# Performance work log

Hardware: AMD Instinct MI355X
Metric: run time of the kernel (lower is better)

The kernel has to match this reference:

```python
import jax, jax.numpy as jnp
import numpy as np

EPS = 1e-5  # 'eps' forward arg, fixed as in typical transformer LayerNorm


def setup_inputs() -> dict:
    key = jax.random.key(0)
    ks = jax.random.split(key, 9)
    B, S, D = 4, 2048, 2048
    scale = 0.02
    return {
        "inputs": jax.random.normal(ks[0], (B, S, D), jnp.float32),
        "norm_weight": jax.random.uniform(ks[1], (D,), jnp.float32),
        "norm_bias": jax.random.normal(ks[2], (D,), jnp.float32) * scale,
        "q_weight": jax.random.normal(ks[3], (D, D), jnp.float32) * scale,
        "q_bias": jax.random.normal(ks[4], (D,), jnp.float32) * scale,
        "k_weight": jax.random.normal(ks[5], (D, D), jnp.float32) * scale,
        "k_bias": jax.random.normal(ks[6], (D,), jnp.float32) * scale,
        "v_weight": jax.random.normal(ks[7], (D, D), jnp.float32) * scale,
        "v_bias": jax.random.normal(ks[8], (D,), jnp.float32) * scale,
        "trans_b": 1,
        "shape_param": 0,
    }


def _layernorm(x, w, b, eps):
    mu = jnp.mean(x, axis=-1, keepdims=True)
    var = jnp.mean(jnp.square(x - mu), axis=-1, keepdims=True)
    return (x - mu) * jax.lax.rsqrt(var + eps) * w + b


def reference(inputs, norm_weight, norm_bias, q_weight, q_bias,
              k_weight, k_bias, v_weight, v_bias, trans_b, shape_param):
    # fused LayerNorm + Q/K/V projection (torch_mlu_ops.fused_norm_attention_project)
    normed = _layernorm(inputs, norm_weight, norm_bias, EPS)
    # trans_b==True convention: weights are [out, in] (nn.Linear layout)
    if not trans_b:
        q_weight = q_weight.T
        k_weight = None if k_weight is None else k_weight.T
        v_weight = None if v_weight is None else v_weight.T
    q = jnp.einsum('bsd,od->bso', normed, q_weight) + q_bias
    outs = [q]
    if k_weight is not None:
        outs.append(jnp.einsum('bsd,od->bso', normed, k_weight) + k_bias)
    if v_weight is not None:
        outs.append(jnp.einsum('bsd,od->bso', normed, v_weight) + v_bias)
    output = jnp.concatenate(outs, axis=-1)  # [B, S, 3*D] fused QKV
    if shape_param:
        output = output.reshape(shape_param)
    return output
```

## Files before the change

kernel.cpp:

```cpp
#include <hip/hip_runtime.h>
#include <hip/hip_bf16.h>
#include <stdint.h>

__device__ __forceinline__ uint16_t f2bf(float f) {
    union { float f; uint32_t u; } c; c.f = f;
    uint32_t u = c.u;
    return (uint16_t)((u + 0x7FFFu + ((u >> 16) & 1u)) >> 16);
}
__device__ __forceinline__ uint32_t pack2(float a, float b) {
    return (uint32_t)f2bf(a) | ((uint32_t)f2bf(b) << 16);
}

typedef __bf16 bf16x8 __attribute__((ext_vector_type(8)));
typedef float  f32x4  __attribute__((ext_vector_type(4)));

#define GLOAD_LDS16(g, l) __builtin_amdgcn_global_load_lds( \
    (const __attribute__((address_space(1))) void*)(g),     \
    (__attribute__((address_space(3))) void*)(l), 16, 0, 0)

#define FENCE() asm volatile("" ::: "memory")

__global__ __launch_bounds__(256) void ln_kernel(
    const float* __restrict__ x, const float* __restrict__ gw,
    const float* __restrict__ gb, uint16_t* __restrict__ y, int D)
{
    const int t = threadIdx.x;
    const size_t row = blockIdx.x;
    const float4* xr = (const float4*)(x + row * (size_t)D);
    float4 v0 = xr[2 * t], v1 = xr[2 * t + 1];

    float s  = v0.x + v0.y + v0.z + v0.w + v1.x + v1.y + v1.z + v1.w;
    float ss = v0.x * v0.x + v0.y * v0.y + v0.z * v0.z + v0.w * v0.w
             + v1.x * v1.x + v1.y * v1.y + v1.z * v1.z + v1.w * v1.w;
#pragma unroll
    for (int off = 32; off > 0; off >>= 1) {
        s  += __shfl_down(s, off);
        ss += __shfl_down(ss, off);
    }
    __shared__ float red[10];
    const int wave = t >> 6, lane = t & 63;
    if (lane == 0) { red[wave] = s; red[4 + wave] = ss; }
    __syncthreads();
    if (t == 0) {
        float S  = red[0] + red[1] + red[2] + red[3];
        float SS = red[4] + red[5] + red[6] + red[7];
        float mu = S / (float)D;
        float var = SS / (float)D - mu * mu;
        red[8] = mu;
        red[9] = rsqrtf(var + 1e-5f);
    }
    __syncthreads();
    const float mu = red[8], rstd = red[9];

    const float4* wr = (const float4*)gw;
    const float4* br = (const float4*)gb;
    float4 w0 = wr[2 * t], w1 = wr[2 * t + 1];
    float4 b0 = br[2 * t], b1 = br[2 * t + 1];

    uint4 ov;
    ov.x = pack2((v0.x - mu) * rstd * w0.x + b0.x, (v0.y - mu) * rstd * w0.y + b0.y);
    ov.y = pack2((v0.z - mu) * rstd * w0.z + b0.z, (v0.w - mu) * rstd * w0.w + b0.w);
    ov.z = pack2((v1.x - mu) * rstd * w1.x + b1.x, (v1.y - mu) * rstd * w1.y + b1.y);
    ov.w = pack2((v1.z - mu) * rstd * w1.z + b1.z, (v1.w - mu) * rstd * w1.w + b1.w);
    ((uint4*)(y + row * (size_t)D))[t] = ov;
}

__global__ __launch_bounds__(256) void wcvt_kernel(
    const float* __restrict__ wq, const float* __restrict__ wk,
    const float* __restrict__ wv, uint16_t* __restrict__ out)
{
    const size_t i = ((size_t)blockIdx.x * 256 + threadIdx.x) * 8;
    const int which = (int)(i >> 22);
    const float* src = (which == 0) ? wq : (which == 1) ? wk : wv;
    const size_t off = i & ((1u << 22) - 1);
    float4 a = *(const float4*)(src + off);
    float4 b = *(const float4*)(src + off + 4);
    uint4 ov;
    ov.x = pack2(a.x, a.y);
    ov.y = pack2(a.z, a.w);
    ov.z = pack2(b.x, b.y);
    ov.w = pack2(b.z, b.w);
    *(uint4*)(out + i) = ov;
}


#define STAGE_A(H, KT, SL) do {                                               \
    const uint16_t* g_ = gA + (size_t)((H) * 128) * K + (KT) * 64;            \
    char* l_ = (char*)lds + (((SL) * 2 + (H)) * 16384) + t * 16;              \
    GLOAD_LDS16(g_, l_);                                                      \
    GLOAD_LDS16(g_ + (size_t)64 * K, l_ + 8192);                              \
} while (0)

#define STAGE_B(H, KT, SL) do {                                               \
    const uint16_t* g_ = gB + (size_t)((H) * 128) * K + (KT) * 64;            \
    char* l_ = (char*)lds + 65536 + (((SL) * 2 + (H)) * 16384) + t * 16;      \
    GLOAD_LDS16(g_, l_);                                                      \
    GLOAD_LDS16(g_ + (size_t)64 * K, l_ + 8192);                              \
} while (0)

#define DS_READ_A(buf, P)                                                     \
    _Pragma("unroll") for (int m_ = 0; m_ < 2; ++m_)                          \
      _Pragma("unroll") for (int s_ = 0; s_ < 2; ++s_)                        \
        buf[m_][s_] = *(const bf16x8*)((const char*)lds + ab_                 \
                                       + (aoff ^ (s_ << 6))                   \
                                       + (2 * (P) + m_) * 2048);

#define DS_READ_BF()                                                          \
    _Pragma("unroll") for (int j_ = 0; j_ < 4; ++j_)                          \
      _Pragma("unroll") for (int s_ = 0; s_ < 2; ++s_)                        \
        Bf[j_][s_] = *(const bf16x8*)((const char*)lds + bb_                  \
                                      + (boff ^ (s_ << 6)) + j_ * 2048);

#define MFMA16(P, buf)                                                        \
    __builtin_amdgcn_s_setprio(1);                                            \
    _Pragma("unroll") for (int s_ = 0; s_ < 2; ++s_)                          \
      _Pragma("unroll") for (int m_ = 0; m_ < 2; ++m_)                        \
        _Pragma("unroll") for (int j_ = 0; j_ < 4; ++j_)                      \
          acc[2 * (P) + m_][j_] = __builtin_amdgcn_mfma_f32_16x16x32_bf16(    \
              buf[m_][s_], Bf[j_][s_], acc[2 * (P) + m_][j_], 0, 0, 0);       \
    __builtin_amdgcn_s_setprio(0);

#define KTILE(SLOT, KT, SA, SB, TAILWAIT)                                     \
  {                                                                           \
    const int ab_ = ((SLOT) * 2 + wr) * 16384;                                \
    const int bb_ = 65536 + ((SLOT) * 2 + (wc >> 1)) * 16384;                 \
    bf16x8 Bf[4][2], AfA[2][2], AfB[2][2];                                    \
                                                                      \
    DS_READ_BF(); DS_READ_A(AfA, 0); DS_READ_A(AfB, 1);                       \
    if (SA) STAGE_A(0, (KT) + 1, (SLOT) ^ 1);                                 \
    FENCE();                                                                  \
    __builtin_amdgcn_s_barrier();                                             \
    MFMA16(0, AfA);                                                           \
    __builtin_amdgcn_s_barrier();                                             \
    FENCE();                                                                  \
                                                                      \
    DS_READ_A(AfA, 2);                                                        \
    if (SA) STAGE_A(1, (KT) + 1, (SLOT) ^ 1);                                 \
    FENCE();                                                                  \
    __builtin_amdgcn_s_barrier();                                             \
    MFMA16(1, AfB);                                                           \
    __builtin_amdgcn_s_barrier();                                             \
    FENCE();                                                                  \
                                                                      \
    DS_READ_A(AfB, 3);                                                        \
    if (SB) STAGE_B(0, (KT) + 2, (SLOT));                                     \
    FENCE();                                                                  \
    __builtin_amdgcn_s_barrier();                                             \
    MFMA16(2, AfA);                                                           \
    __builtin_amdgcn_s_barrier();                                             \
    FENCE();                                                                  \
                                                                      \
    if (SB) STAGE_B(1, (KT) + 2, (SLOT));                                     \
    FENCE();                                                                  \
    __builtin_amdgcn_s_barrier();                                             \
    MFMA16(3, AfB);                                                           \
    TAILWAIT                                                                  \
    __builtin_amdgcn_s_barrier();                                             \
    FENCE();                                                                  \
  }

__global__ __launch_bounds__(512, 2) void qkv_gemm256(
    const uint16_t* __restrict__ A, const uint16_t* __restrict__ W,
    const float* __restrict__ Bq, const float* __restrict__ Bk,
    const float* __restrict__ Bv, float* __restrict__ C,
    int M, int N, int K)
{
    (void)M;
    extern __shared__ uint16_t lds[];
    const int t = threadIdx.x;
    const int lane = t & 63, wid = t >> 6;
    const int wr = wid >> 2, wc = wid & 3;
    const int fr = lane & 15;
    const int fq2 = (lane >> 4) * 16;

    const int nbt = N >> 8;
    const int nwg = gridDim.x;
    int mb, nb;
    if ((nwg & 7) == 0) {
        const int cpx = nwg >> 3;
        const int xcd = blockIdx.x & 7, ti = blockIdx.x >> 3;
        if (cpx % nbt == 0 && (nbt & 7) == 0) {
            const int band = ti >> 5, r = ti & 31;
            mb = xcd * (cpx / nbt) + (r >> 3);
            nb = (band << 3) + (r & 7);
        } else {
            const int swz = xcd * cpx + ti;
            mb = swz / nbt; nb = swz % nbt;
        }
    } else {
        mb = blockIdx.x / nbt; nb = blockIdx.x % nbt;
    }

    const int kbase = fq2 ^ ((fr & 7) << 4);
    const int aoff = fr * 128 + kbase;
    const int boff = ((wc & 1) * 64 + fr) * 128 + kbase;

    const int srow = t >> 3;
    const int scol = (((t & 7) ^ ((t >> 3) & 7)) << 3);
    const uint16_t* gA = A + (size_t)(mb * 256 + srow) * K + scol;
    const uint16_t* gB = W + (size_t)(nb * 256 + srow) * K + scol;

    f32x4 acc[8][4] = {};
    const int NT = K >> 6;

    STAGE_B(0, 0, 0); STAGE_B(1, 0, 0);
    STAGE_A(0, 0, 0); STAGE_A(1, 0, 0);
    STAGE_B(0, 1, 1); STAGE_B(1, 1, 1);
    asm volatile("s_waitcnt vmcnt(4)" ::: "memory");
    __builtin_amdgcn_s_barrier();
    FENCE();

#pragma unroll 1
    for (int i = 0; i < (NT >> 1) - 1; ++i) {
        const int k0 = i << 1;
        KTILE(0, k0,     1, 1, asm volatile("s_waitcnt vmcnt(4)" ::: "memory");)
        KTILE(1, k0 + 1, 1, 1, asm volatile("s_waitcnt vmcnt(4)" ::: "memory");)
    }
    KTILE(0, NT - 2, 1, 0, asm volatile("s_waitcnt vmcnt(0)" ::: "memory");)
    KTILE(1, NT - 1, 0, 0, )

    const int r0 = mb * 256 + wr * 128 + (lane >> 4) * 4;
    const int c0 = nb * 256 + wc * 64 + fr;
    const float* bp = (nb < 8) ? Bq : (nb < 16) ? Bk : Bv;
    const int cb = (nb & 7) * 256 + wc * 64 + fr;
    float bj[4];
#pragma unroll
    for (int j = 0; j < 4; ++j) bj[j] = bp[cb + j * 16];
#pragma unroll
    for (int i = 0; i < 8; ++i)
#pragma unroll
        for (int j = 0; j < 4; ++j)
#pragma unroll
            for (int r = 0; r < 4; ++r)
                C[(size_t)(r0 + i * 16 + r) * N + c0 + j * 16] = acc[i][j][r] + bj[j];
}

extern "C" void kernel_launch(void* const* d_in, const int* in_sizes, int n_in,
                              void* d_out, int out_size, void* d_ws, size_t ws_size,
                              hipStream_t stream) {
    const float* x  = (const float*)d_in[0];
    const float* nw = (const float*)d_in[1];
    const float* nb = (const float*)d_in[2];
    const float* wq = (const float*)d_in[3];
    const float* bq = (const float*)d_in[4];
    const float* wk = (const float*)d_in[5];
    const float* bk = (const float*)d_in[6];
    const float* wv = (const float*)d_in[7];
    const float* bv = (const float*)d_in[8];

    const int D = in_sizes[1];
    const int M = in_sizes[0] / D;
    const int N = 3 * D;

    static bool attr_done = false;
    if (!attr_done) {
        hipFuncSetAttribute((const void*)qkv_gemm256,
                            hipFuncAttributeMaxDynamicSharedMemorySize, 131072);
        attr_done = true;
    }

    uint16_t* normed = (uint16_t*)d_ws;
    uint16_t* wcat   = normed + (size_t)M * D;

    ln_kernel<<<M, 256, 0, stream>>>(x, nw, nb, normed, D);
    wcvt_kernel<<<((size_t)N * D) / (256 * 8), 256, 0, stream>>>(wq, wk, wv, wcat);
    const int grid = (M / 256) * (N / 256);
    qkv_gemm256<<<grid, 512, 131072, stream>>>(normed, wcat, bq, bk, bv,
                                               (float*)d_out, M, N, D);
}
```

Measured before the change: 457.9 us.

## Software-pipeline LDS fragment reads across k-tiles with double-buffered B registers

Restructures the GEMM k-tile loop so each tile's LDS reads happen during the previous quarter's MFMAs. The next tile's B fragments and first A fragments are prefetched into alternating register sets (BfA/BfB). Barriers per tile drop from eight to four, and vmcnt waits are redistributed to expose more overlap between LDS reads, global-to-LDS loads and MFMA. This raises register pressure under launch_bounds(512,2) and risks LDS read/write hazards if the wait placement is wrong.

```diff
diff --git a/kernel.cpp b/kernel.cpp
--- a/kernel.cpp
+++ b/kernel.cpp
@@ -19,6 +19,7 @@
     (__attribute__((address_space(3))) void*)(l), 16, 0, 0)
 
 #define FENCE() asm volatile("" ::: "memory")
+#define SCHEDB() __builtin_amdgcn_sched_barrier(0)
 
 __global__ __launch_bounds__(256) void ln_kernel(
     const float* __restrict__ x, const float* __restrict__ gw,
@@ -98,66 +99,61 @@
     GLOAD_LDS16(g_ + (size_t)64 * K, l_ + 8192);                              \
 } while (0)
 
-#define DS_READ_A(buf, P)                                                     \
+#define DS_READ_Q(buf, P, ABASE)                                              \
     _Pragma("unroll") for (int m_ = 0; m_ < 2; ++m_)                          \
       _Pragma("unroll") for (int s_ = 0; s_ < 2; ++s_)                        \
-        buf[m_][s_] = *(const bf16x8*)((const char*)lds + ab_                 \
+        buf[m_][s_] = *(const bf16x8*)((const char*)lds + (ABASE)             \
                                        + (aoff ^ (s_ << 6))                   \
                                        + (2 * (P) + m_) * 2048);
 
-#define DS_READ_BF()                                                          \
+#define DS_READ_B(BF, BBASE)                                                  \
     _Pragma("unroll") for (int j_ = 0; j_ < 4; ++j_)                          \
       _Pragma("unroll") for (int s_ = 0; s_ < 2; ++s_)                        \
-        Bf[j_][s_] = *(const bf16x8*)((const char*)lds + bb_                  \
+        BF[j_][s_] = *(const bf16x8*)((const char*)lds + (BBASE)              \
                                       + (boff ^ (s_ << 6)) + j_ * 2048);
 
-#define MFMA16(P, buf)                                                        \
+#define MFMA16(P, buf, BF)                                                    \
     __builtin_amdgcn_s_setprio(1);                                            \
     _Pragma("unroll") for (int s_ = 0; s_ < 2; ++s_)                          \
       _Pragma("unroll") for (int m_ = 0; m_ < 2; ++m_)                        \
         _Pragma("unroll") for (int j_ = 0; j_ < 4; ++j_)                      \
           acc[2 * (P) + m_][j_] = __builtin_amdgcn_mfma_f32_16x16x32_bf16(    \
-              buf[m_][s_], Bf[j_][s_], acc[2 * (P) + m_][j_], 0, 0, 0);       \
+              buf[m_][s_], BF[j_][s_], acc[2 * (P) + m_][j_], 0, 0, 0);       \
     __builtin_amdgcn_s_setprio(0);
 
-#define KTILE(SLOT, KT, SA, SB, TAILWAIT)                                     \
+#define KTILE(SLOT, KT, BFC, BFN, SA, SB, PFN, VM1, VM2)                      \
   {                                                                           \
-    const int ab_ = ((SLOT) * 2 + wr) * 16384;                                \
-    const int bb_ = 65536 + ((SLOT) * 2 + (wc >> 1)) * 16384;                 \
-    bf16x8 Bf[4][2], AfA[2][2], AfB[2][2];                                    \
-                                                                      \
-    DS_READ_BF(); DS_READ_A(AfA, 0); DS_READ_A(AfB, 1);                       \
+    const int ab_  = ((SLOT) * 2 + wr) * 16384;                               \
+    const int abn_ = (((SLOT) ^ 1) * 2 + wr) * 16384;                         \
+    const int bbn_ = 65536 + (((SLOT) ^ 1) * 2 + (wc >> 1)) * 16384;          \
+                                                                      \
     if (SA) STAGE_A(0, (KT) + 1, (SLOT) ^ 1);                                 \
-    FENCE();                                                                  \
-    __builtin_amdgcn_s_barrier();                                             \
-    MFMA16(0, AfA);                                                           \
-    __builtin_amdgcn_s_barrier();                                             \
-    FENCE();                                                                  \
-                                                                      \
-    DS_READ_A(AfA, 2);                                                        \
+    MFMA16(0, Xq, BFC);                                                       \
+    DS_READ_Q(Xq, 2, ab_);                                                    \
+    FENCE(); __builtin_amdgcn_s_barrier(); FENCE();                           \
+                                                                      \
     if (SA) STAGE_A(1, (KT) + 1, (SLOT) ^ 1);                                 \
-    FENCE();                                                                  \
-    __builtin_amdgcn_s_barrier();                                             \
-    MFMA16(1, AfB);                                                           \
-    __builtin_amdgcn_s_barrier();                                             \
-    FENCE();                                                                  \
-                                                                      \
-    DS_READ_A(AfB, 3);                                                        \
+    MFMA16(1, Yq, BFC);                                                       \
+    DS_READ_Q(Yq, 3, ab_);                                                    \
+    VM1 FENCE(); __builtin_amdgcn_s_barrier(); FENCE();                       \
+                                                                      \
+    if (PFN) { DS_READ_B(BFN, bbn_); }                                        \
     if (SB) STAGE_B(0, (KT) + 2, (SLOT));                                     \
-    FENCE();                                                                  \
-    __builtin_amdgcn_s_barrier();                                             \
-    MFMA16(2, AfA);                                                           \
-    __builtin_amdgcn_s_barrier();                                             \
-    FENCE();                                                                  \
-                                                                      \
+    SCHEDB();                                                                 \
+    MFMA16(2, Xq, BFC);                                                       \
+    VM2 FENCE(); __builtin_amdgcn_s_barrier(); FENCE();                       \
+                                                                      \
+    if (PFN) { DS_READ_Q(Xq, 0, abn_); }                                      \
     if (SB) STAGE_B(1, (KT) + 2, (SLOT));                                     \
-    FENCE();                                                                  \
-    __builtin_amdgcn_s_barrier();                                             \
-    MFMA16(3, AfB);                                                           \
-    TAILWAIT                                                                  \
-    __builtin_amdgcn_s_barrier();                                             \
-    FENCE();                                                                  \
+    SCHEDB();                                                                 \
+    MFMA16(3, Yq, BFC);                                                       \
+    if (PFN) { DS_READ_Q(Yq, 1, abn_); }                                      \
+    FENCE(); __builtin_amdgcn_s_barrier(); FENCE();                           \
   }
+
+#define VM4 asm volatile("s_waitcnt vmcnt(4)" ::: "memory");
+#define VM2W asm volatile("s_waitcnt vmcnt(2)" ::: "memory");
+#define VM0 asm volatile("s_waitcnt vmcnt(0)" ::: "memory");
 
 __global__ __launch_bounds__(512, 2) void qkv_gemm256(
     const uint16_t* __restrict__ A, const uint16_t* __restrict__ W,
@@ -201,23 +197,32 @@
     const uint16_t* gB = W + (size_t)(nb * 256 + srow) * K + scol;
 
     f32x4 acc[8][4] = {};
+    bf16x8 Xq[2][2], Yq[2][2], BfA[4][2], BfB[4][2];
     const int NT = K >> 6;
 
     STAGE_B(0, 0, 0); STAGE_B(1, 0, 0);
     STAGE_A(0, 0, 0); STAGE_A(1, 0, 0);
     STAGE_B(0, 1, 1); STAGE_B(1, 1, 1);
-    asm volatile("s_waitcnt vmcnt(4)" ::: "memory");
+    VM4
     __builtin_amdgcn_s_barrier();
+    FENCE();
+    {
+        const int ab_ = wr * 16384;
+        const int bb_ = 65536 + (wc >> 1) * 16384;
+        DS_READ_B(BfA, bb_);
+        DS_READ_Q(Xq, 0, ab_);
+        DS_READ_Q(Yq, 1, ab_);
+    }
     FENCE();
 
 #pragma unroll 1
     for (int i = 0; i < (NT >> 1) - 1; ++i) {
         const int k0 = i << 1;
-        KTILE(0, k0,     1, 1, asm volatile("s_waitcnt vmcnt(4)" ::: "memory");)
-        KTILE(1, k0 + 1, 1, 1, asm volatile("s_waitcnt vmcnt(4)" ::: "memory");)
-    }
-    KTILE(0, NT - 2, 1, 0, asm volatile("s_waitcnt vmcnt(0)" ::: "memory");)
-    KTILE(1, NT - 1, 0, 0, )
+        KTILE(0, k0,     BfA, BfB, 1, 1, 1, VM4, VM2W)
+        KTILE(1, k0 + 1, BfB, BfA, 1, 1, 1, VM4, VM2W)
+    }
+    KTILE(0, NT - 2, BfA, BfB, 1, 0, 1, VM4, VM0)
+    KTILE(1, NT - 1, BfB, BfA, 0, 0, 0, , )
 
     const int r0 = mb * 256 + wr * 128 + (lane >> 4) * 4;
     const int c0 = nb * 256 + wc * 64 + fr;
```

Result: slower. 758.4 us (+65.6%).
